# Kernel tuning notes

Hardware: AMD Instinct MI355X
Metric: run time of the kernel (lower is better)

The kernel has to match this reference:

```python
import jax, jax.numpy as jnp
import numpy as np

B, S, D_IN = 2, 2048, 2048
H, G, HD = 16, 4, 128          # num_heads, num_kv_groups, head_dim
GROUP = H // G                  # 4 query heads per kv group
D_OUT = H * HD                  # 2048
EPS = 1e-6


def _rope_tables(seq_len, head_dim, theta=10000.0):
    inv = 1.0 / (theta ** (np.arange(0, head_dim, 2, dtype=np.float32) / head_dim))
    pos = np.arange(seq_len, dtype=np.float32)
    ang = np.outer(pos, inv)                      # [S, HD/2]
    ang = np.concatenate([ang, ang], axis=-1)     # [S, HD]
    return jnp.asarray(np.cos(ang)), jnp.asarray(np.sin(ang))


def setup_inputs() -> dict:
    key = jax.random.key(0)
    ks = jax.random.split(key, 6)
    x = jax.random.normal(ks[0], (B, S, D_IN), dtype=jnp.float32)
    # Linear weights stored as [in, out] so y = x @ W (same math as nn.Linear)
    Wq = jax.random.normal(ks[1], (D_IN, 2 * D_OUT), dtype=jnp.float32) * (D_IN ** -0.5)
    Wk = jax.random.normal(ks[2], (D_IN, G * HD), dtype=jnp.float32) * (D_IN ** -0.5)
    Wv = jax.random.normal(ks[3], (D_IN, G * HD), dtype=jnp.float32) * (D_IN ** -0.5)
    Wo = jax.random.normal(ks[4], (D_OUT, D_IN), dtype=jnp.float32) * (D_OUT ** -0.5)
    q_norm_w = jnp.zeros((HD,), dtype=jnp.float32)  # Qwen-style zero-init (scale = 1 + w)
    k_norm_w = jnp.zeros((HD,), dtype=jnp.float32)
    cos, sin = _rope_tables(S, HD)
    mask = jnp.triu(jnp.ones((S, S), dtype=bool), k=1)  # causal: True above diagonal is masked
    return {"x": x, "Wq": Wq, "Wk": Wk, "Wv": Wv, "Wo": Wo,
            "q_norm_w": q_norm_w, "k_norm_w": k_norm_w,
            "cos": cos, "sin": sin, "mask": mask}


def _rmsnorm(x, w):
    xf = x.astype(jnp.float32)
    n = xf * jax.lax.rsqrt(jnp.mean(xf * xf, axis=-1, keepdims=True) + EPS)
    return (n * (1.0 + w.astype(jnp.float32))).astype(x.dtype)


def _apply_rope(x, cos, sin):
    # x: [..., S, HD]; full-dim rotation (rot_dim == head_dim)
    s = x.shape[-2]
    c = cos[:s][None, None]
    sn = sin[:s][None, None]
    x1, x2 = x[..., : HD // 2], x[..., HD // 2 :]
    rotated = jnp.concatenate([-x2, x1], axis=-1)
    return (x * c + rotated * sn).astype(x.dtype)


def reference(x, Wq, Wk, Wv, Wo, q_norm_w, k_norm_w, cos, sin, mask):
    b, s, _ = x.shape
    qg = (x @ Wq).reshape(b, s, H, 2 * HD)
    q, gate = qg[..., :HD], qg[..., HD:]
    gate = gate.reshape(b, s, D_OUT)
    q = q.transpose(0, 2, 1, 3)                                 # [b,H,s,HD]
    k = (x @ Wk).reshape(b, s, G, HD).transpose(0, 2, 1, 3)     # [b,G,s,HD]
    v = (x @ Wv).reshape(b, s, G, HD).transpose(0, 2, 1, 3)
    q = _rmsnorm(q, q_norm_w)
    k = _rmsnorm(k, k_norm_w)
    q = _apply_rope(q, cos, sin)
    k = _apply_rope(k, cos, sin)
    # GQA: group query heads by kv group instead of repeat_interleave on k/v
    qg4 = q.reshape(b, G, GROUP, s, HD)
    scores = jnp.einsum("bgjqd,bgkd->bgjqk", qg4, k)            # [b,G,GROUP,s,s]
    scores = jnp.where(mask[None, None, None], -jnp.inf, scores)
    w = jax.nn.softmax((scores * (HD ** -0.5)).astype(jnp.float32), axis=-1).astype(q.dtype)
    ctx = jnp.einsum("bgjqk,bgkd->bgjqd", w, v)                 # [b,G,GROUP,s,HD]
    ctx = ctx.reshape(b, H, s, HD).transpose(0, 2, 1, 3).reshape(b, s, D_OUT)
    ctx = ctx * jax.nn.sigmoid(gate)
    return ctx @ Wo
```

## Files before the change

kernel.cpp:

```cpp
#include <hip/hip_runtime.h>

#define S_LEN 2048
#define NROWS 4096
#define DIN   2048
#define DQKV  5120
#define DQG   4096

typedef __bf16 bf16x8 __attribute__((ext_vector_type(8)));
typedef float  floatx4 __attribute__((ext_vector_type(4)));
typedef unsigned short u16;

#define QK_SCALE 0.08838834764831845f

__device__ __forceinline__ u16 f2bf(float f) {
  unsigned int u = __float_as_uint(f);
  u += 0x7fffu + ((u >> 16) & 1u);
  return (u16)(u >> 16);
}
__device__ __forceinline__ float bf2f(u16 v) {
  return __uint_as_float(((unsigned int)v) << 16);
}
__device__ __forceinline__ int swz(int col, int row) {
  return (col & ~63) | ((((col >> 3) & 7) ^ (row & 7)) << 3) | (col & 7);
}

__device__ __forceinline__ void gload_lds16(const void* g, void* l) {
  __builtin_amdgcn_global_load_lds(
      (__attribute__((address_space(1))) void*)(void*)(g),
      (__attribute__((address_space(3))) void*)(l), 16, 0, 0);
}

__global__ __launch_bounds__(256) void cvt_x(const float* __restrict__ src,
                                             u16* __restrict__ dst) {
  const int i = blockIdx.x * 256 + threadIdx.x;
  const int row = i >> 9, col = (i & 511) << 2;
  const float4 v = reinterpret_cast<const float4*>(src)[i];
  ushort4 o;
  o.x = f2bf(v.x); o.y = f2bf(v.y); o.z = f2bf(v.z); o.w = f2bf(v.w);
  *reinterpret_cast<ushort4*>(dst + (size_t)row * DIN + swz(col, row)) = o;
}

__global__ __launch_bounds__(256) void tcvt(const float* __restrict__ src,
                                            u16* __restrict__ dst,
                                            int R, int C, int dld) {
  __shared__ float tile[32][33];
  const int c0 = blockIdx.x * 32, r0 = blockIdx.y * 32;
  const int t = threadIdx.x;
  {
    const int rl = t >> 3, cl4 = (t & 7) * 4;
    const float4 v = *reinterpret_cast<const float4*>(src + (size_t)(r0 + rl) * C + c0 + cl4);
    tile[rl][cl4 + 0] = v.x; tile[rl][cl4 + 1] = v.y;
    tile[rl][cl4 + 2] = v.z; tile[rl][cl4 + 3] = v.w;
  }
  __syncthreads();
  {
    const int cl = t >> 3, rl4 = (t & 7) * 4;
    ushort4 o;
    o.x = f2bf(tile[rl4 + 0][cl]); o.y = f2bf(tile[rl4 + 1][cl]);
    o.z = f2bf(tile[rl4 + 2][cl]); o.w = f2bf(tile[rl4 + 3][cl]);
    const int rd = c0 + cl, cd = r0 + rl4;
    *reinterpret_cast<ushort4*>(dst + (size_t)rd * dld + swz(cd, rd)) = o;
  }
}

template <bool BF16_OUT>
__global__ __launch_bounds__(256) void gemm_bt(const u16* __restrict__ A,
                                               const u16* __restrict__ Bt,
                                               void* __restrict__ Cv,
                                               int M, int N, int K, int ldc) {
  __shared__ __align__(16) u16 As[128 * 64];
  __shared__ __align__(16) u16 Bs[128 * 64];
  const int tid = threadIdx.x, wv = tid >> 6, lane = tid & 63;
  const int m0 = blockIdx.y * 128, n0 = blockIdx.x * 128;
  const int wm = (wv >> 1) * 64, wn = (wv & 1) * 64;
  const int frow = lane & 15, quad = lane >> 4, fsw = frow & 7;
  const int srow = lane >> 3, scol = (lane & 7) * 8;
  floatx4 acc[4][4] = {};
  for (int k0 = 0; k0 < K; k0 += 64) {
#pragma unroll
    for (int i = 0; i < 4; ++i) {
      const int rr = (wv * 4 + i) * 8;
      gload_lds16(A  + (size_t)(m0 + rr + srow) * K + k0 + scol, &As[rr * 64]);
      gload_lds16(Bt + (size_t)(n0 + rr + srow) * K + k0 + scol, &Bs[rr * 64]);
    }
    __syncthreads();
#pragma unroll
    for (int ks = 0; ks < 2; ++ks) {
      bf16x8 af[4], bfr[4];
#pragma unroll
      for (int mi = 0; mi < 4; ++mi)
        af[mi] = *reinterpret_cast<const bf16x8*>(
            &As[(wm + mi * 16 + frow) * 64 + (((ks * 4 + quad) ^ fsw) << 3)]);
#pragma unroll
      for (int ni = 0; ni < 4; ++ni)
        bfr[ni] = *reinterpret_cast<const bf16x8*>(
            &Bs[(wn + ni * 16 + frow) * 64 + (((ks * 4 + quad) ^ fsw) << 3)]);
#pragma unroll
      for (int mi = 0; mi < 4; ++mi)
#pragma unroll
        for (int ni = 0; ni < 4; ++ni)
          acc[mi][ni] = __builtin_amdgcn_mfma_f32_16x16x32_bf16(af[mi], bfr[ni], acc[mi][ni], 0, 0, 0);
    }
    __syncthreads();
  }
  const int crow = (lane >> 4) * 4, ccol = lane & 15;
#pragma unroll
  for (int mi = 0; mi < 4; ++mi)
#pragma unroll
    for (int ni = 0; ni < 4; ++ni) {
      const size_t base = (size_t)(m0 + wm + mi * 16 + crow) * ldc + (n0 + wn + ni * 16 + ccol);
      if constexpr (BF16_OUT) {
        u16* C = (u16*)Cv;
#pragma unroll
        for (int r = 0; r < 4; ++r) C[base + (size_t)r * ldc] = f2bf(acc[mi][ni][r]);
      } else {
        float* C = (float*)Cv;
#pragma unroll
        for (int r = 0; r < 4; ++r) C[base + (size_t)r * ldc] = acc[mi][ni][r];
      }
    }
}

__global__ __launch_bounds__(512, 2) void gemm256(const u16* __restrict__ A,
                                                  const u16* __restrict__ Bt,
                                                  u16* __restrict__ C,
                                                  int K, int ldc) {
  __shared__ __align__(16) u16 As[2][256 * 64];
  __shared__ __align__(16) u16 Bs[2][256 * 64];
  const int tid = threadIdx.x, wv = tid >> 6, lane = tid & 63;
  const int nx = gridDim.x;
  const int orig = blockIdx.y * nx + blockIdx.x;
  const int cpx = (nx * gridDim.y) >> 3;
  const int wgid = (orig & 7) * cpx + (orig >> 3);
  const int m0 = (wgid / nx) * 256, n0 = (wgid % nx) * 256;
  const int wm = (wv >> 2) * 128, wn = (wv & 3) * 64;
  const int f = lane & 15, quad = lane >> 4, fs = f & 7;

  const u16* Ab = A  + (size_t)(m0 + wv * 8 + (lane >> 3)) * K + (lane & 7) * 8;
  const u16* Bb = Bt + (size_t)(n0 + wv * 8 + (lane >> 3)) * K + (lane & 7) * 8;

  floatx4 acc[8][4] = {};
  bf16x8 af[4], bfr[4];

  auto stageA = [&](int sl, int t, int u) {
    gload_lds16(Ab + (size_t)u * 64 * K + (size_t)t * 64, &As[sl][(u * 64 + wv * 8) * 64]);
  };
  auto stageB = [&](int sl, int t, int u) {
    gload_lds16(Bb + (size_t)u * 64 * K + (size_t)t * 64, &Bs[sl][(u * 64 + wv * 8) * 64]);
  };
  auto loadA = [&](int sl, int fh, int ks) {
#pragma unroll
    for (int mf = 0; mf < 4; ++mf)
      af[mf] = *reinterpret_cast<const bf16x8*>(
          &As[sl][(wm + fh * 64 + mf * 16 + f) * 64 + ((((ks << 2) + quad) ^ fs) << 3)]);
  };
  auto loadB = [&](int sl, int ks) {
#pragma unroll
    for (int nf = 0; nf < 4; ++nf)
      bfr[nf] = *reinterpret_cast<const bf16x8*>(
          &Bs[sl][(wn + nf * 16 + f) * 64 + ((((ks << 2) + quad) ^ fs) << 3)]);
  };
  auto mmas = [&](int fh) {
#pragma unroll
    for (int mf = 0; mf < 4; ++mf)
#pragma unroll
      for (int nf = 0; nf < 4; ++nf)
        acc[fh * 4 + mf][nf] = __builtin_amdgcn_mfma_f32_16x16x32_bf16(
            af[mf], bfr[nf], acc[fh * 4 + mf][nf], 0, 0, 0);
  };

#pragma unroll
  for (int u = 0; u < 4; ++u) stageA(0, 0, u);
#pragma unroll
  for (int u = 0; u < 4; ++u) stageB(0, 0, u);
  stageA(1, 1, 0); stageA(1, 1, 2); stageB(1, 1, 0);
  asm volatile("s_waitcnt vmcnt(3)" ::: "memory");
  __builtin_amdgcn_s_barrier();

  const int IT = K >> 7;
#pragma unroll 1
  for (int i = 0; i < IT; ++i) {
    const int t0 = 2 * i;
    const bool st = (i < IT - 1);
    loadA(0, 0, 0); loadB(0, 0);
    stageA(1, t0 + 1, 1); stageA(1, t0 + 1, 3); stageB(1, t0 + 1, 1);
    __builtin_amdgcn_s_barrier();
    asm volatile("s_waitcnt lgkmcnt(0)" ::: "memory");
    __builtin_amdgcn_s_setprio(1); mmas(0); __builtin_amdgcn_s_setprio(0);
    __builtin_amdgcn_s_barrier();
    loadA(0, 1, 0);
    stageB(1, t0 + 1, 2); stageB(1, t0 + 1, 3);
    __builtin_amdgcn_s_barrier();
    asm volatile("s_waitcnt lgkmcnt(0)" ::: "memory");
    __builtin_amdgcn_s_setprio(1); mmas(1); __builtin_amdgcn_s_setprio(0);
    __builtin_amdgcn_s_barrier();
    loadA(0, 0, 1); loadB(0, 1);
    __builtin_amdgcn_s_barrier();
    asm volatile("s_waitcnt lgkmcnt(0)" ::: "memory");
    __builtin_amdgcn_s_setprio(1); mmas(0); __builtin_amdgcn_s_setprio(0);
    __builtin_amdgcn_s_barrier();
    loadA(0, 1, 1);
    if (st) { stageA(0, t0 + 2, 0); stageA(0, t0 + 2, 2); stageB(0, t0 + 2, 0); }
    __builtin_amdgcn_s_barrier();
    asm volatile("s_waitcnt lgkmcnt(0)" ::: "memory");
    __builtin_amdgcn_s_setprio(1); mmas(1); __builtin_amdgcn_s_setprio(0);
    if (st) { asm volatile("s_waitcnt vmcnt(3)" ::: "memory"); }
    else    { asm volatile("s_waitcnt vmcnt(0)" ::: "memory"); }
    __builtin_amdgcn_s_barrier();
    loadA(1, 0, 0); loadB(1, 0);
    if (st) { stageA(0, t0 + 2, 1); stageA(0, t0 + 2, 3); stageB(0, t0 + 2, 1); }
    __builtin_amdgcn_s_barrier();
    asm volatile("s_waitcnt lgkmcnt(0)" ::: "memory");
    __builtin_amdgcn_s_setprio(1); mmas(0); __builtin_amdgcn_s_setprio(0);
    __builtin_amdgcn_s_barrier();
    loadA(1, 1, 0);
    if (st) { stageB(0, t0 + 2, 2); stageB(0, t0 + 2, 3); }
    __builtin_amdgcn_s_barrier();
    asm volatile("s_waitcnt lgkmcnt(0)" ::: "memory");
    __builtin_amdgcn_s_setprio(1); mmas(1); __builtin_amdgcn_s_setprio(0);
    __builtin_amdgcn_s_barrier();
    loadA(1, 0, 1); loadB(1, 1);
    __builtin_amdgcn_s_barrier();
    asm volatile("s_waitcnt lgkmcnt(0)" ::: "memory");
    __builtin_amdgcn_s_setprio(1); mmas(0); __builtin_amdgcn_s_setprio(0);
    __builtin_amdgcn_s_barrier();
    loadA(1, 1, 1);
    if (st) { stageA(1, t0 + 3, 0); stageA(1, t0 + 3, 2); stageB(1, t0 + 3, 0); }
    __builtin_amdgcn_s_barrier();
    asm volatile("s_waitcnt lgkmcnt(0)" ::: "memory");
    __builtin_amdgcn_s_setprio(1); mmas(1); __builtin_amdgcn_s_setprio(0);
    if (st) { asm volatile("s_waitcnt vmcnt(3)" ::: "memory"); }
    __builtin_amdgcn_s_barrier();
  }

#pragma unroll
  for (int mf = 0; mf < 8; ++mf)
#pragma unroll
    for (int nf = 0; nf < 4; ++nf) {
      const size_t base = (size_t)(m0 + wm + (mf >> 2) * 64 + (mf & 3) * 16 + quad * 4) * ldc
                        + (n0 + wn + nf * 16 + f);
#pragma unroll
      for (int r = 0; r < 4; ++r) C[base + (size_t)r * ldc] = f2bf(acc[mf][nf][r]);
    }
}

__global__ __launch_bounds__(256) void qnorm_rope(const u16* __restrict__ QKV,
                                                  const float* __restrict__ w,
                                                  const float* __restrict__ cosT,
                                                  const float* __restrict__ sinT,
                                                  u16* __restrict__ Qb) {
  const int wv = threadIdx.x >> 6, lane = threadIdx.x & 63;
  const int idx = blockIdx.x * 4 + wv;
  const int h = idx & 15, row = idx >> 4;
  const int s = row & (S_LEN - 1), b = row >> 11;
  const u16* base = QKV + (size_t)row * DQKV + h * 256;
  const float v0 = bf2f(base[lane]), v1 = bf2f(base[lane + 64]);
  float ss = v0 * v0 + v1 * v1;
#pragma unroll
  for (int m = 32; m >= 1; m >>= 1) ss += __shfl_xor(ss, m);
  const float rn = rsqrtf(ss * (1.0f / 128.0f) + 1e-6f) * QK_SCALE;
  const float n0 = v0 * rn * (1.0f + w[lane]);
  const float n1 = v1 * rn * (1.0f + w[lane + 64]);
  const float c0 = cosT[(size_t)s * 128 + lane], c1 = cosT[(size_t)s * 128 + lane + 64];
  const float sn0 = sinT[(size_t)s * 128 + lane], sn1 = sinT[(size_t)s * 128 + lane + 64];
  u16* qb = Qb + ((size_t)(b * 16 + h) * S_LEN + s) * 128;
  qb[lane]      = f2bf(n0 * c0 - n1 * sn0);
  qb[lane + 64] = f2bf(n1 * c1 + n0 * sn1);
}

__global__ __launch_bounds__(256) void knorm_rope(const u16* __restrict__ QKV,
                                                  const float* __restrict__ w,
                                                  const float* __restrict__ cosT,
                                                  const float* __restrict__ sinT,
                                                  u16* __restrict__ Kb) {
  const int wv = threadIdx.x >> 6, lane = threadIdx.x & 63;
  const int idx = blockIdx.x * 4 + wv;
  const int g = idx & 3, row = idx >> 2;
  const int s = row & (S_LEN - 1), b = row >> 11;
  const u16* base = QKV + (size_t)row * DQKV + DQG + g * 128;
  const float v0 = bf2f(base[lane]), v1 = bf2f(base[lane + 64]);
  float ss = v0 * v0 + v1 * v1;
#pragma unroll
  for (int m = 32; m >= 1; m >>= 1) ss += __shfl_xor(ss, m);
  const float rn = rsqrtf(ss * (1.0f / 128.0f) + 1e-6f);
  const float n0 = v0 * rn * (1.0f + w[lane]);
  const float n1 = v1 * rn * (1.0f + w[lane + 64]);
  const float c0 = cosT[(size_t)s * 128 + lane], c1 = cosT[(size_t)s * 128 + lane + 64];
  const float sn0 = sinT[(size_t)s * 128 + lane], sn1 = sinT[(size_t)s * 128 + lane + 64];
  u16* kb = Kb + ((size_t)(b * 4 + g) * S_LEN + s) * 128;
  const int sw = s & 7;
  const int d0 = lane, d1 = lane + 64;
  const int p0 = (((d0 >> 3) ^ sw) << 3) | (d0 & 7);
  const int p1 = (((d1 >> 3) ^ sw) << 3) | (d1 & 7);
  kb[p0] = f2bf(n0 * c0 - n1 * sn0);
  kb[p1] = f2bf(n1 * c1 + n0 * sn1);
}

__global__ __launch_bounds__(256) void vtrans(const u16* __restrict__ QKV,
                                              u16* __restrict__ Vt) {
  __shared__ u16 tile[32][40];
  const int bg = blockIdx.z;
  const int s0 = blockIdx.x * 32, d0 = blockIdx.y * 32;
  const int b = bg >> 2, g = bg & 3;
  const int t = threadIdx.x;
  {
    const int sl = t >> 3, dl4 = (t & 7) * 4;
    const ushort4 v = *reinterpret_cast<const ushort4*>(
        QKV + (size_t)(b * S_LEN + s0 + sl) * DQKV + DQG + 512 + g * 128 + d0 + dl4);
    tile[sl][dl4 + 0] = v.x; tile[sl][dl4 + 1] = v.y;
    tile[sl][dl4 + 2] = v.z; tile[sl][dl4 + 3] = v.w;
  }
  __syncthreads();
  {
    const int dl = t >> 3, sl4 = (t & 7) * 4;
    ushort4 o;
    o.x = tile[sl4 + 0][dl]; o.y = tile[sl4 + 1][dl];
    o.z = tile[sl4 + 2][dl]; o.w = tile[sl4 + 3][dl];
    const int d = d0 + dl, s = s0 + sl4;
    const size_t base = (size_t)(bg * 128 + d) * S_LEN + (s & ~63);
    const int pos = ((((s >> 3) & 7) ^ (d & 7)) << 3) | (s & 7);
    *reinterpret_cast<ushort4*>(Vt + base + pos) = o;
  }
}

__global__ __launch_bounds__(256) void attn(const u16* __restrict__ Qb,
                                            const u16* __restrict__ Kb,
                                            const u16* __restrict__ Vt,
                                            const u16* __restrict__ QKV,
                                            u16* __restrict__ ctxg) {
  __shared__ __align__(16) u16 Ks[2][64 * 128];
  __shared__ __align__(16) u16 Vts[2][128 * 64];
  __shared__ __align__(16) u16 Ps[4][16 * 68];
  const int tid = threadIdx.x, wv = tid >> 6, lane = tid & 63;
  const int ip = blockIdx.x, bh = blockIdx.y;
  const int b = bh >> 4, h = bh & 15, g = h >> 2, bg = b * 4 + g;
  const int f = lane & 15, quad = lane >> 4, fq = quad * 8;
  const int fsw = f & 7;
  const u16* Kp = Kb + (size_t)bg * S_LEN * 128;
  const u16* Vp = Vt + (size_t)bg * 128 * S_LEN;
  u16* Pw = Ps[wv];

  auto stage_kv = [&](int sl, int kt) {
    const int k0 = kt * 64;
#pragma unroll
    for (int i = 0; i < 4; ++i) {
      const int j = wv * 4 + i;
      gload_lds16(Kp + (size_t)k0 * 128 + j * 512 + lane * 8, &Ks[sl][j * 512]);
    }
#pragma unroll
    for (int i = 0; i < 4; ++i) {
      const int r0 = (wv * 4 + i) * 8;
      gload_lds16(Vp + (size_t)(r0 + (lane >> 3)) * S_LEN + k0 + (lane & 7) * 8,
                  &Vts[sl][r0 * 64]);
    }
  };

  for (int pass = 0; pass < 2; ++pass) {
    const int qt = pass ? 31 - ip : ip;
    const u16* Qp = Qb + ((size_t)bh * S_LEN + qt * 64 + wv * 16) * 128;
    bf16x8 aq[4];
#pragma unroll
    for (int c = 0; c < 4; ++c)
      aq[c] = *reinterpret_cast<const bf16x8*>(&Qp[(size_t)f * 128 + c * 32 + fq]);

    floatx4 o[8] = {};
    float lsum[4] = {0.f, 0.f, 0.f, 0.f};
    const int nkt = qt + 1;

    stage_kv(0, 0);
    asm volatile("s_waitcnt vmcnt(0)" ::: "memory");
    __syncthreads();

    int cur = 0;
    for (int kt = 0; kt < nkt; ++kt) {
      const int k0 = kt * 64;
      if (kt + 1 < nkt) stage_kv(cur ^ 1, kt + 1);

      floatx4 sc[4] = {};
#pragma unroll
      for (int c = 0; c < 4; ++c) {
#pragma unroll
        for (int n = 0; n < 4; ++n) {
          bf16x8 bk = *reinterpret_cast<const bf16x8*>(
              &Ks[cur][(n * 16 + f) * 128 + (((4 * c + quad) ^ fsw) << 3)]);
          sc[n] = __builtin_amdgcn_mfma_f32_16x16x32_bf16(aq[c], bk, sc[n], 0, 0, 0);
        }
      }

      const int qrow0 = qt * 64 + wv * 16 + quad * 4;
#pragma unroll
      for (int n = 0; n < 4; ++n) {
        const int key = k0 + n * 16 + f;
#pragma unroll
        for (int r = 0; r < 4; ++r) {
          const float p = (key <= qrow0 + r) ? __expf(sc[n][r]) : 0.f;
          lsum[r] += p;
          Pw[(quad * 4 + r) * 68 + n * 16 + f] = f2bf(p);
        }
      }

#pragma unroll
      for (int kf = 0; kf < 2; ++kf) {
        bf16x8 pf = *reinterpret_cast<const bf16x8*>(&Pw[f * 68 + kf * 32 + fq]);
#pragma unroll
        for (int dt = 0; dt < 8; ++dt) {
          bf16x8 bv = *reinterpret_cast<const bf16x8*>(
              &Vts[cur][(dt * 16 + f) * 64 + (((4 * kf + quad) ^ fsw) << 3)]);
          o[dt] = __builtin_amdgcn_mfma_f32_16x16x32_bf16(pf, bv, o[dt], 0, 0, 0);
        }
      }

      asm volatile("s_waitcnt vmcnt(0)" ::: "memory");
      __syncthreads();
      cur ^= 1;
    }

#pragma unroll
    for (int r = 0; r < 4; ++r) {
#pragma unroll
      for (int mm = 8; mm >= 1; mm >>= 1) lsum[r] += __shfl_xor(lsum[r], mm);
    }

#pragma unroll
    for (int r = 0; r < 4; ++r) {
      const int s = qt * 64 + wv * 16 + quad * 4 + r;
      const size_t grow = (size_t)b * S_LEN + s;
      const float inv = 1.0f / lsum[r];
#pragma unroll
      for (int dt = 0; dt < 8; ++dt) {
        const int d = dt * 16 + f;
        const float gate = bf2f(QKV[grow * DQKV + h * 256 + 128 + d]);
        const float val = o[dt][r] * inv * (1.0f / (1.0f + __expf(-gate)));
        const int col = h * 128 + d;
        ctxg[grow * 2048 + swz(col, (int)grow)] = f2bf(val);
      }
    }
  }
}

extern "C" void kernel_launch(void* const* d_in, const int* in_sizes, int n_in,
                              void* d_out, int out_size, void* d_ws, size_t ws_size,
                              hipStream_t stream) {
  const float* x    = (const float*)d_in[0];
  const float* Wq   = (const float*)d_in[1];
  const float* Wk   = (const float*)d_in[2];
  const float* Wv   = (const float*)d_in[3];
  const float* Wo   = (const float*)d_in[4];
  const float* qnw  = (const float*)d_in[5];
  const float* knw  = (const float*)d_in[6];
  const float* cosT = (const float*)d_in[7];
  const float* sinT = (const float*)d_in[8];

  char* p = (char*)d_ws;
  u16*   xb    = (u16*)p;  p += (size_t)NROWS * DIN * 2;
  u16*   WqkvT = (u16*)p;  p += (size_t)DQKV * DIN * 2;
  u16*   WoT   = (u16*)p;  p += (size_t)2048 * 2048 * 2;
  u16*   QKVb  = (u16*)p;  p += (size_t)NROWS * DQKV * 2;
  u16*   Qbf   = (u16*)p;  p += (size_t)2 * 16 * S_LEN * 128 * 2;
  u16*   Kbf   = (u16*)p;  p += (size_t)2 * 4 * S_LEN * 128 * 2;
  u16*   Vtb   = (u16*)p;  p += (size_t)2 * 4 * S_LEN * 128 * 2;
  u16*   ctxg  = (u16*)p;  p += (size_t)NROWS * 2048 * 2;

  cvt_x<<<8192, 256, 0, stream>>>(x, xb);
  tcvt<<<dim3(128, 64), 256, 0, stream>>>(Wq, WqkvT, 2048, 4096, 2048);
  tcvt<<<dim3(16, 64), 256, 0, stream>>>(Wk, WqkvT + (size_t)4096 * 2048, 2048, 512, 2048);
  tcvt<<<dim3(16, 64), 256, 0, stream>>>(Wv, WqkvT + (size_t)4608 * 2048, 2048, 512, 2048);
  tcvt<<<dim3(64, 64), 256, 0, stream>>>(Wo, WoT, 2048, 2048, 2048);

  gemm256<<<dim3(16, 16), 512, 0, stream>>>(xb, WqkvT, QKVb, DIN, DQKV);
  gemm_bt<true><<<dim3(8, 32), 256, 0, stream>>>(
      xb, WqkvT + (size_t)4096 * 2048, QKVb + 4096, NROWS, 1024, DIN, DQKV);

  qnorm_rope<<<16384, 256, 0, stream>>>(QKVb, qnw, cosT, sinT, Qbf);
  knorm_rope<<<4096, 256, 0, stream>>>(QKVb, knw, cosT, sinT, Kbf);
  vtrans<<<dim3(64, 4, 8), 256, 0, stream>>>(QKVb, Vtb);

  attn<<<dim3(16, 32), 256, 0, stream>>>(Qbf, Kbf, Vtb, QKVb, ctxg);

  gemm_bt<false><<<dim3(16, 32), 256, 0, stream>>>(ctxg, WoT, (float*)d_out, NROWS, 2048, 2048, 2048);
}
```

Baseline: 412.9 us.

## Software-pipeline QK^T of next tile with PV of current tile in attention

Restructures the attention inner loop so the QK^T MFMAs and exp for tile t+1 are computed while the PV MFMAs for tile t run. K and V loads are split and issued at different points with partial vmcnt waits, which keeps more loads in flight. The score MFMA operands are swapped so each lane holds one query row, giving a single lsum per lane and vectorized P stores into an XOR-swizzled unpadded LDS buffer. The cost is more live registers for the extra score accumulators and an extra barrier per iteration.

```diff
diff --git a/kernel.cpp b/kernel.cpp
--- a/kernel.cpp
+++ b/kernel.cpp
@@ -330,7 +330,7 @@
                                             u16* __restrict__ ctxg) {
   __shared__ __align__(16) u16 Ks[2][64 * 128];
   __shared__ __align__(16) u16 Vts[2][128 * 64];
-  __shared__ __align__(16) u16 Ps[4][16 * 68];
+  __shared__ __align__(16) u16 Ps[4][16 * 64];
   const int tid = threadIdx.x, wv = tid >> 6, lane = tid & 63;
   const int ip = blockIdx.x, bh = blockIdx.y;
   const int b = bh >> 4, h = bh & 15, g = h >> 2, bg = b * 4 + g;
@@ -339,14 +339,20 @@
   const u16* Kp = Kb + (size_t)bg * S_LEN * 128;
   const u16* Vp = Vt + (size_t)bg * 128 * S_LEN;
   u16* Pw = Ps[wv];
-
-  auto stage_kv = [&](int sl, int kt) {
+  const int pwr_base = f * 64 + ((quad & 1) << 2);
+  const int pf0_off = f * 64 + ((quad ^ fsw) << 3);
+  const int pf1_off = f * 64 + (((4 + quad) ^ fsw) << 3);
+
+  auto stage_k = [&](int sl, int kt) {
     const int k0 = kt * 64;
 #pragma unroll
     for (int i = 0; i < 4; ++i) {
       const int j = wv * 4 + i;
       gload_lds16(Kp + (size_t)k0 * 128 + j * 512 + lane * 8, &Ks[sl][j * 512]);
     }
+  };
+  auto stage_v = [&](int sl, int kt) {
+    const int k0 = kt * 64;
 #pragma unroll
     for (int i = 0; i < 4; ++i) {
       const int r0 = (wv * 4 + i) * 8;
@@ -357,6 +363,7 @@
 
   for (int pass = 0; pass < 2; ++pass) {
     const int qt = pass ? 31 - ip : ip;
+    const int qrow = qt * 64 + wv * 16 + f;
     const u16* Qp = Qb + ((size_t)bh * S_LEN + qt * 64 + wv * 16) * 128;
     bf16x8 aq[4];
 #pragma unroll
@@ -364,73 +371,120 @@
       aq[c] = *reinterpret_cast<const bf16x8*>(&Qp[(size_t)f * 128 + c * 32 + fq]);
 
     floatx4 o[8] = {};
-    float lsum[4] = {0.f, 0.f, 0.f, 0.f};
+    float lsum = 0.f;
     const int nkt = qt + 1;
 
-    stage_kv(0, 0);
-    asm volatile("s_waitcnt vmcnt(0)" ::: "memory");
     __syncthreads();
-
-    int cur = 0;
-    for (int kt = 0; kt < nkt; ++kt) {
-      const int k0 = kt * 64;
-      if (kt + 1 < nkt) stage_kv(cur ^ 1, kt + 1);
-
+    stage_k(0, 0); stage_v(0, 0);
+    if (nkt > 1) {
+      stage_k(1, 1); stage_v(1, 1);
+      asm volatile("s_waitcnt vmcnt(8)" ::: "memory");
+    } else {
+      asm volatile("s_waitcnt vmcnt(0)" ::: "memory");
+    }
+    __syncthreads();
+
+    {
       floatx4 sc[4] = {};
 #pragma unroll
-      for (int c = 0; c < 4; ++c) {
+      for (int c = 0; c < 4; ++c)
 #pragma unroll
         for (int n = 0; n < 4; ++n) {
           bf16x8 bk = *reinterpret_cast<const bf16x8*>(
-              &Ks[cur][(n * 16 + f) * 128 + (((4 * c + quad) ^ fsw) << 3)]);
-          sc[n] = __builtin_amdgcn_mfma_f32_16x16x32_bf16(aq[c], bk, sc[n], 0, 0, 0);
+              &Ks[0][(n * 16 + f) * 128 + (((4 * c + quad) ^ fsw) << 3)]);
+          sc[n] = __builtin_amdgcn_mfma_f32_16x16x32_bf16(bk, aq[c], sc[n], 0, 0, 0);
         }
-      }
-
-      const int qrow0 = qt * 64 + wv * 16 + quad * 4;
 #pragma unroll
       for (int n = 0; n < 4; ++n) {
-        const int key = k0 + n * 16 + f;
+        float pv_[4];
 #pragma unroll
         for (int r = 0; r < 4; ++r) {
-          const float p = (key <= qrow0 + r) ? __expf(sc[n][r]) : 0.f;
-          lsum[r] += p;
-          Pw[(quad * 4 + r) * 68 + n * 16 + f] = f2bf(p);
+          const int key = n * 16 + quad * 4 + r;
+          const float p = (key <= qrow) ? __expf(sc[n][r]) : 0.f;
+          lsum += p; pv_[r] = p;
         }
-      }
-
-#pragma unroll
-      for (int kf = 0; kf < 2; ++kf) {
-        bf16x8 pf = *reinterpret_cast<const bf16x8*>(&Pw[f * 68 + kf * 32 + fq]);
-#pragma unroll
-        for (int dt = 0; dt < 8; ++dt) {
-          bf16x8 bv = *reinterpret_cast<const bf16x8*>(
-              &Vts[cur][(dt * 16 + f) * 64 + (((4 * kf + quad) ^ fsw) << 3)]);
-          o[dt] = __builtin_amdgcn_mfma_f32_16x16x32_bf16(pf, bv, o[dt], 0, 0, 0);
+        ushort4 pk;
+        pk.x = f2bf(pv_[0]); pk.y = f2bf(pv_[1]); pk.z = f2bf(pv_[2]); pk.w = f2bf(pv_[3]);
+        *reinterpret_cast<ushort4*>(
+            &Pw[pwr_base + (((2 * n + (quad >> 1)) ^ fsw) << 3)]) = pk;
+      }
+    }
+    if (nkt > 1) {
+      asm volatile("s_waitcnt vmcnt(4)" ::: "memory");
+      __syncthreads();
+    }
+
+    int cur = 0;
+    for (int t = 0; t < nkt; ++t) {
+      const bool more = (t + 1 < nkt);
+      floatx4 sn[4] = {};
+      if (more) {
+#pragma unroll
+        for (int c = 0; c < 4; ++c)
+#pragma unroll
+          for (int n = 0; n < 4; ++n) {
+            bf16x8 bk = *reinterpret_cast<const bf16x8*>(
+                &Ks[cur ^ 1][(n * 16 + f) * 128 + (((4 * c + quad) ^ fsw) << 3)]);
+            sn[n] = __builtin_amdgcn_mfma_f32_16x16x32_bf16(bk, aq[c], sn[n], 0, 0, 0);
+          }
+        if (t + 2 < nkt) stage_k(cur, t + 2);
+      }
+      bf16x8 pf0 = *reinterpret_cast<const bf16x8*>(&Pw[pf0_off]);
+      bf16x8 pf1 = *reinterpret_cast<const bf16x8*>(&Pw[pf1_off]);
+#pragma unroll
+      for (int dt = 0; dt < 8; ++dt) {
+        bf16x8 bv = *reinterpret_cast<const bf16x8*>(
+            &Vts[cur][(dt * 16 + f) * 64 + ((quad ^ fsw) << 3)]);
+        o[dt] = __builtin_amdgcn_mfma_f32_16x16x32_bf16(pf0, bv, o[dt], 0, 0, 0);
+      }
+#pragma unroll
+      for (int dt = 0; dt < 8; ++dt) {
+        bf16x8 bv = *reinterpret_cast<const bf16x8*>(
+            &Vts[cur][(dt * 16 + f) * 64 + (((4 + quad) ^ fsw) << 3)]);
+        o[dt] = __builtin_amdgcn_mfma_f32_16x16x32_bf16(pf1, bv, o[dt], 0, 0, 0);
+      }
+      if (more) {
+        const int kb = (t + 1) * 64;
+#pragma unroll
+        for (int n = 0; n < 4; ++n) {
+          float pv_[4];
+#pragma unroll
+          for (int r = 0; r < 4; ++r) {
+            const int key = kb + n * 16 + quad * 4 + r;
+            const float p = (key <= qrow) ? __expf(sn[n][r]) : 0.f;
+            lsum += p; pv_[r] = p;
+          }
+          ushort4 pk;
+          pk.x = f2bf(pv_[0]); pk.y = f2bf(pv_[1]); pk.z = f2bf(pv_[2]); pk.w = f2bf(pv_[3]);
+          *reinterpret_cast<ushort4*>(
+              &Pw[pwr_base + (((2 * n + (quad >> 1)) ^ fsw) << 3)]) = pk;
         }
-      }
-
-      asm volatile("s_waitcnt vmcnt(0)" ::: "memory");
-      __syncthreads();
-      cur ^= 1;
-    }
+        __syncthreads();
+        if (t + 2 < nkt) {
+          stage_v(cur, t + 2);
+          asm volatile("s_waitcnt vmcnt(4)" ::: "memory");
+        } else {
+          asm volatile("s_waitcnt vmcnt(0)" ::: "memory");
+        }
+        __syncthreads();
+        cur ^= 1;
+      }
+    }
+
+    lsum += __shfl_xor(lsum, 16);
+    lsum += __shfl_xor(lsum, 32);
+    const float inv = 1.0f / lsum;
 
 #pragma unroll
     for (int r = 0; r < 4; ++r) {
-#pragma unroll
-      for (int mm = 8; mm >= 1; mm >>= 1) lsum[r] += __shfl_xor(lsum[r], mm);
-    }
-
-#pragma unroll
-    for (int r = 0; r < 4; ++r) {
+      const float linv = __shfl(inv, quad * 4 + r);
       const int s = qt * 64 + wv * 16 + quad * 4 + r;
       const size_t grow = (size_t)b * S_LEN + s;
-      const float inv = 1.0f / lsum[r];
 #pragma unroll
       for (int dt = 0; dt < 8; ++dt) {
         const int d = dt * 16 + f;
         const float gate = bf2f(QKV[grow * DQKV + h * 256 + 128 + d]);
-        const float val = o[dt][r] * inv * (1.0f / (1.0f + __expf(-gate)));
+        const float val = o[dt][r] * linv * (1.0f / (1.0f + __expf(-gate)));
         const int col = h * 128 + d;
         ctxg[grow * 2048 + swz(col, (int)grow)] = f2bf(val);
       }
```

After: 408.9 us. Within noise of the previous version (-1.0%).
